# Kernel tuning notes

Hardware: AMD Instinct MI355X
Metric: run time of the kernel (lower is better)

Reference implementation:

```python
import jax, jax.numpy as jnp
import numpy as np
from jax import lax

B, L, DM = 2, 1024, 1024
DIN, DSTATE, DCONV, DTRANK = 2048, 16, 4, 64


def setup_inputs() -> dict:
    key = jax.random.key(0)
    ks = jax.random.split(key, 8)
    s = 0.02
    x = jax.random.normal(ks[0], (B, L, DM), jnp.float32)
    in_proj_w = jax.random.normal(ks[1], (2 * DIN, DM), jnp.float32) * s
    conv_w = jax.random.normal(ks[2], (DIN, 1, DCONV), jnp.float32) * 0.2
    conv_b = jnp.zeros((DIN,), jnp.float32)
    x_proj_w = jax.random.normal(ks[3], (DTRANK + 2 * DSTATE, DIN), jnp.float32) * s
    dt_proj_w = jax.random.normal(ks[4], (DIN, DTRANK), jnp.float32) * s
    dt_proj_b = jnp.full((DIN,), -4.0, jnp.float32)  # small init dt after softplus
    # S4D-real init: A_log = log(1..d_state) per channel
    A_log = jnp.log(jnp.broadcast_to(jnp.arange(1, DSTATE + 1, dtype=jnp.float32), (DIN, DSTATE)))
    D_skip = jnp.ones((DIN,), jnp.float32)
    out_proj_w = jax.random.normal(ks[5], (DM, DIN), jnp.float32) * s
    return {
        "x": x, "norm_w": jnp.ones((DM,), jnp.float32), "norm_b": jnp.zeros((DM,), jnp.float32),
        "in_proj_w": in_proj_w, "conv_w": conv_w, "conv_b": conv_b,
        "x_proj_w": x_proj_w, "dt_proj_w": dt_proj_w, "dt_proj_b": dt_proj_b,
        "A_log": A_log, "D_skip": D_skip, "out_proj_w": out_proj_w,
    }


def _layernorm(x, w, b, eps=1e-5):
    mu = jnp.mean(x, axis=-1, keepdims=True)
    var = jnp.mean(jnp.square(x - mu), axis=-1, keepdims=True)
    return (x - mu) * lax.rsqrt(var + eps) * w + b


def _mamba(h, in_proj_w, conv_w, conv_b, x_proj_w, dt_proj_w, dt_proj_b, A_log, D_skip, out_proj_w):
    # h: [B, L, DM]
    xz = jnp.einsum('bld,ed->ble', h, in_proj_w)          # [B, L, 2*DIN]
    xm, z = jnp.split(xz, 2, axis=-1)                     # each [B, L, DIN]
    # causal depthwise conv1d over time
    xc = jnp.transpose(xm, (0, 2, 1))                     # [B, DIN, L]
    xc = jnp.pad(xc, ((0, 0), (0, 0), (DCONV - 1, 0)))
    xc = lax.conv_general_dilated(xc, conv_w, (1,), 'VALID',
                                  dimension_numbers=('NCH', 'OIH', 'NCH'),
                                  feature_group_count=DIN)
    xc = xc + conv_b[None, :, None]
    xc = jnp.transpose(xc, (0, 2, 1))                     # [B, L, DIN]
    xc = jax.nn.silu(xc)
    # input-dependent SSM parameters
    x_dbl = jnp.einsum('bld,ed->ble', xc, x_proj_w)       # [B, L, DTRANK+2N]
    dt, Bm, Cm = jnp.split(x_dbl, [DTRANK, DTRANK + DSTATE], axis=-1)
    dt = jax.nn.softplus(jnp.einsum('blr,dr->bld', dt, dt_proj_w) + dt_proj_b)  # [B, L, DIN]
    A = -jnp.exp(A_log)                                   # [DIN, N]
    deltaA = jnp.exp(dt[..., None] * A)                   # [B, L, DIN, N]
    deltaBu = dt[..., None] * Bm[:, :, None, :] * xc[..., None]  # [B, L, DIN, N]
    # sequential selective scan over time
    dA_t = jnp.transpose(deltaA, (1, 0, 2, 3))            # [L, B, DIN, N]
    dBu_t = jnp.transpose(deltaBu, (1, 0, 2, 3))
    C_t = jnp.transpose(Cm, (1, 0, 2))                    # [L, B, N]

    def step(hs, inp):
        dA, dBu, Ct = inp
        hs = dA * hs + dBu                                # [B, DIN, N]
        y = jnp.einsum('bdn,bn->bd', hs, Ct)
        return hs, y

    h0 = jnp.zeros((B, DIN, DSTATE), xc.dtype)
    _, ys = lax.scan(step, h0, (dA_t, dBu_t, C_t))        # ys: [L, B, DIN]
    y = jnp.transpose(ys, (1, 0, 2)) + xc * D_skip        # [B, L, DIN]
    y = y * jax.nn.silu(z)
    return jnp.einsum('bld,ed->ble', y, out_proj_w)       # [B, L, DM]


def reference(x, norm_w, norm_b, in_proj_w, conv_w, conv_b, x_proj_w,
              dt_proj_w, dt_proj_b, A_log, D_skip, out_proj_w):
    h = _layernorm(x, norm_w, norm_b)
    return x + _mamba(h, in_proj_w, conv_w, conv_b, x_proj_w,
                      dt_proj_w, dt_proj_b, A_log, D_skip, out_proj_w)
```

## Files before the change

kernel.cpp:

```cpp
#include <hip/hip_runtime.h>


typedef unsigned short u16;
typedef unsigned int u32;

typedef __bf16 bf16x8 __attribute__((ext_vector_type(8)));
typedef float f32x4 __attribute__((ext_vector_type(4)));

#define SCAN_G 32
#define SCAN_T 32
#define NSTATE 65536

#if __has_builtin(__builtin_amdgcn_exp2f)
#define EXP2F(x) __builtin_amdgcn_exp2f(x)
#else
#define EXP2F(x) exp2f(x)
#endif
#define LOG2E 1.44269504f

__device__ __forceinline__ u16 f2bf(float f) {
  u32 u = __float_as_uint(f);
  u32 r = u + 0x7FFFu + ((u >> 16) & 1u);
  return (u16)(r >> 16);
}
__device__ __forceinline__ float bf2f(u16 v) {
  return __uint_as_float(((u32)v) << 16);
}

__device__ __forceinline__ void lds_load16(const u16* g, u16* l) {
  __builtin_amdgcn_global_load_lds(
      (const __attribute__((address_space(1))) u32*)g,
      (__attribute__((address_space(3))) u32*)l, 16, 0, 0);
}

__global__ __launch_bounds__(256) void convert_ln_kernel(
    const float* __restrict__ w0, const float* __restrict__ w1,
    const float* __restrict__ w2, const float* __restrict__ w3,
    u16* __restrict__ o0, u16* __restrict__ o1,
    u16* __restrict__ o2, u16* __restrict__ o3,
    const float* __restrict__ x, const float* __restrict__ nw,
    const float* __restrict__ nb, u16* __restrict__ h) {
  const int bx = blockIdx.x;
  const int tid = threadIdx.x;
  if (bx < 25856) {
    const int i = bx * 256 + tid;
    if (i < 4194304) {
      o0[i] = f2bf(w0[i]);
    } else if (i < 4390912) {
      const int j = i - 4194304;
      o1[j] = f2bf(w1[j]);
    } else if (i < 4521984) {
      const int j = i - 4390912;
      o2[j] = f2bf(w2[j]);
    } else if (i < 6619136) {
      const int j = i - 4521984;
      o3[j] = f2bf(w3[j]);
    }
    return;
  }
  const int row = bx - 25856;
  const float4 v = ((const float4*)(x + (size_t)row * 1024))[tid];
  float s = v.x + v.y + v.z + v.w;
  float s2 = v.x * v.x + v.y * v.y + v.z * v.z + v.w * v.w;
  for (int off = 32; off >= 1; off >>= 1) {
    s += __shfl_xor(s, off);
    s2 += __shfl_xor(s2, off);
  }
  __shared__ float red[8];
  const int wave = tid >> 6;
  if ((tid & 63) == 0) { red[wave * 2] = s; red[wave * 2 + 1] = s2; }
  __syncthreads();
  s = red[0] + red[2] + red[4] + red[6];
  s2 = red[1] + red[3] + red[5] + red[7];
  const float mu = s * (1.0f / 1024.0f);
  const float var = s2 * (1.0f / 1024.0f) - mu * mu;
  const float rstd = rsqrtf(var + 1e-5f);
  const float4 wv = ((const float4*)nw)[tid];
  const float4 bv = ((const float4*)nb)[tid];
  ushort4 o;
  o.x = f2bf((v.x - mu) * rstd * wv.x + bv.x);
  o.y = f2bf((v.y - mu) * rstd * wv.y + bv.y);
  o.z = f2bf((v.z - mu) * rstd * wv.z + bv.z);
  o.w = f2bf((v.w - mu) * rstd * wv.w + bv.w);
  ((ushort4*)(h + (size_t)row * 1024))[tid] = o;
}

__global__ __launch_bounds__(256) void gemm_bt_kernel(
    const u16* __restrict__ A, const u16* __restrict__ W,
    float* __restrict__ C, int M, int N, int K) {
  const int n0 = blockIdx.x * 64;
  const int m0 = blockIdx.y * 64;
  const int ks = blockIdx.z;
  const int kLen = K / 4;
  const int kOff = ks * kLen;
  __shared__ u16 As[64 * 32];
  __shared__ u16 Ws[64 * 32];
  const int tid = threadIdx.x;
  const int wave = tid >> 6;
  const int lane = tid & 63;
  const int wm = (wave >> 1) * 32;
  const int wn = (wave & 1) * 32;
  const int lrow = tid >> 2;
  const int lcg = (tid & 3) * 8;
  const int arow = m0 + lrow;
  const int wrow = n0 + lrow;
  f32x4 acc[2][2];
#pragma unroll
  for (int i = 0; i < 2; ++i)
#pragma unroll
    for (int j = 0; j < 2; ++j) acc[i][j] = (f32x4){0.f, 0.f, 0.f, 0.f};

  const int fm = lane & 15;
  const int fk = (lane >> 4) * 8;

  for (int k0 = kOff; k0 < kOff + kLen; k0 += 32) {
    uint4 av = *(const uint4*)(A + (size_t)arow * K + k0 + lcg);
    uint4 wv = make_uint4(0u, 0u, 0u, 0u);
    if (wrow < N) wv = *(const uint4*)(W + (size_t)wrow * K + k0 + lcg);
    __syncthreads();
    *(uint4*)(As + lrow * 32 + lcg) = av;
    *(uint4*)(Ws + lrow * 32 + lcg) = wv;
    __syncthreads();
    bf16x8 a0 = *(const bf16x8*)(As + (wm + fm) * 32 + fk);
    bf16x8 a1 = *(const bf16x8*)(As + (wm + 16 + fm) * 32 + fk);
    bf16x8 b0 = *(const bf16x8*)(Ws + (wn + fm) * 32 + fk);
    bf16x8 b1 = *(const bf16x8*)(Ws + (wn + 16 + fm) * 32 + fk);
    acc[0][0] = __builtin_amdgcn_mfma_f32_16x16x32_bf16(a0, b0, acc[0][0], 0, 0, 0);
    acc[0][1] = __builtin_amdgcn_mfma_f32_16x16x32_bf16(a0, b1, acc[0][1], 0, 0, 0);
    acc[1][0] = __builtin_amdgcn_mfma_f32_16x16x32_bf16(a1, b0, acc[1][0], 0, 0, 0);
    acc[1][1] = __builtin_amdgcn_mfma_f32_16x16x32_bf16(a1, b1, acc[1][1], 0, 0, 0);
  }

  const int col = lane & 15;
  const int rbase = (lane >> 4) * 4;
#pragma unroll
  for (int tm = 0; tm < 2; ++tm)
#pragma unroll
    for (int tn = 0; tn < 2; ++tn)
#pragma unroll
      for (int r = 0; r < 4; ++r) {
        int m = m0 + wm + tm * 16 + rbase + r;
        int n = n0 + wn + tn * 16 + col;
        if (n < N)
          C[(size_t)ks * M * N + (size_t)m * N + n] = acc[tm][tn][r];
      }
}

__global__ __launch_bounds__(256) void dtgemm_fused_kernel(
    const float* __restrict__ xpart, const u16* __restrict__ Wdt,
    const float* __restrict__ bias, const u16* __restrict__ xcb,
    u32* __restrict__ dxp, float* __restrict__ xdbl) {
  const int N = 2048, K = 64;
  const int n0 = blockIdx.x * 64;
  const int m0 = blockIdx.y * 64;
  const int tid = threadIdx.x;

  if (blockIdx.x == 0) {
#pragma unroll
    for (int j = 0; j < 8; ++j) {
      const int e = tid * 8 + j;
      const int r = e >> 5, c = e & 31;
      const size_t ix = (size_t)(m0 + r) * 96 + 64 + c;
      xdbl[ix] = xpart[ix] + xpart[ix + 196608] + xpart[ix + 2 * 196608] +
                 xpart[ix + 3 * 196608];
    }
  }

  __shared__ u16 As[64 * 32];
  __shared__ u16 Ws[64 * 32];
  const int wave = tid >> 6;
  const int lane = tid & 63;
  const int wm = (wave >> 1) * 32;
  const int wn = (wave & 1) * 32;
  const int lrow = tid >> 2;
  const int lcg = (tid & 3) * 8;
  f32x4 acc[2][2];
#pragma unroll
  for (int i = 0; i < 2; ++i)
#pragma unroll
    for (int j = 0; j < 2; ++j) acc[i][j] = (f32x4){0.f, 0.f, 0.f, 0.f};

  const int fm = lane & 15;
  const int fk = (lane >> 4) * 8;

  for (int k0 = 0; k0 < K; k0 += 32) {
    const size_t ab = (size_t)(m0 + lrow) * 96 + k0 + lcg;
    float av[8];
#pragma unroll
    for (int t = 0; t < 2; ++t) {
      float4 v0 = *(const float4*)&xpart[ab + t * 4];
      float4 v1 = *(const float4*)&xpart[ab + 196608 + t * 4];
      float4 v2 = *(const float4*)&xpart[ab + 2 * 196608 + t * 4];
      float4 v3 = *(const float4*)&xpart[ab + 3 * 196608 + t * 4];
      av[t * 4 + 0] = v0.x + v1.x + v2.x + v3.x;
      av[t * 4 + 1] = v0.y + v1.y + v2.y + v3.y;
      av[t * 4 + 2] = v0.z + v1.z + v2.z + v3.z;
      av[t * 4 + 3] = v0.w + v1.w + v2.w + v3.w;
    }
    ushort4 ap0, ap1;
    ap0.x = f2bf(av[0]); ap0.y = f2bf(av[1]); ap0.z = f2bf(av[2]); ap0.w = f2bf(av[3]);
    ap1.x = f2bf(av[4]); ap1.y = f2bf(av[5]); ap1.z = f2bf(av[6]); ap1.w = f2bf(av[7]);
    uint4 wv = *(const uint4*)(Wdt + (size_t)(n0 + lrow) * K + k0 + lcg);
    __syncthreads();
    *(ushort4*)(As + lrow * 32 + lcg) = ap0;
    *(ushort4*)(As + lrow * 32 + lcg + 4) = ap1;
    *(uint4*)(Ws + lrow * 32 + lcg) = wv;
    __syncthreads();
    bf16x8 a0 = *(const bf16x8*)(As + (wm + fm) * 32 + fk);
    bf16x8 a1 = *(const bf16x8*)(As + (wm + 16 + fm) * 32 + fk);
    bf16x8 b0 = *(const bf16x8*)(Ws + (wn + fm) * 32 + fk);
    bf16x8 b1 = *(const bf16x8*)(Ws + (wn + 16 + fm) * 32 + fk);
    acc[0][0] = __builtin_amdgcn_mfma_f32_16x16x32_bf16(a0, b0, acc[0][0], 0, 0, 0);
    acc[0][1] = __builtin_amdgcn_mfma_f32_16x16x32_bf16(a0, b1, acc[0][1], 0, 0, 0);
    acc[1][0] = __builtin_amdgcn_mfma_f32_16x16x32_bf16(a1, b0, acc[1][0], 0, 0, 0);
    acc[1][1] = __builtin_amdgcn_mfma_f32_16x16x32_bf16(a1, b1, acc[1][1], 0, 0, 0);
  }

  const int col = lane & 15;
  const int rbase = (lane >> 4) * 4;
#pragma unroll
  for (int tm = 0; tm < 2; ++tm)
#pragma unroll
    for (int tn = 0; tn < 2; ++tn)
#pragma unroll
      for (int r = 0; r < 4; ++r) {
        const int m = m0 + wm + tm * 16 + rbase + r;
        const int n = n0 + wn + tn * 16 + col;
        float v = acc[tm][tn][r] + bias[n];
        v = (v > 20.f) ? v : log1pf(__expf(v));
        const u32 xc = xcb[(size_t)m * 2048 + n];
        dxp[(size_t)m * 2048 + n] = (u32)f2bf(v) | (xc << 16);
      }
}

template <int EPI, int SPLITK>
__global__ __launch_bounds__(256) void gemm128_kernel(
    const u16* __restrict__ A, const u16* __restrict__ W,
    u16* __restrict__ Cout, int M, int N, int K) {
  const int n0 = blockIdx.x * 128;
  const int m0 = blockIdx.y * 128;
  const int ks = (SPLITK > 1) ? blockIdx.z : 0;
  const int kLen = K / SPLITK;
  const int k0 = ks * kLen;
  __shared__ u16 As[128 * 32];
  __shared__ u16 Ws[128 * 32];
  const int tid = threadIdx.x;
  const int wave = tid >> 6;
  const int lane = tid & 63;
  const int wm = (wave >> 1) * 64;
  const int wn = (wave & 1) * 64;
  f32x4 acc[4][4];
#pragma unroll
  for (int i = 0; i < 4; ++i)
#pragma unroll
    for (int j = 0; j < 4; ++j) acc[i][j] = (f32x4){0.f, 0.f, 0.f, 0.f};

  const int fm = lane & 15;
  const int fk = (lane >> 4) * 8;
  const int sr = lane >> 2;
  const int sc = (lane & 3) * 8;
  const u16* gA = A + (size_t)(m0 + wave * 32 + sr) * K + k0 + sc;
  const u16* gB = W + (size_t)(n0 + wave * 32 + sr) * K + k0 + sc;
  u16* lA = As + wave * 1024;
  u16* lB = Ws + wave * 1024;

  for (int kk = 0; kk < kLen; kk += 32) {
    __syncthreads();
    lds_load16(gA + kk, lA);
    lds_load16(gA + (size_t)16 * K + kk, lA + 512);
    lds_load16(gB + kk, lB);
    lds_load16(gB + (size_t)16 * K + kk, lB + 512);
    __syncthreads();
    bf16x8 af[4], bfr[4];
#pragma unroll
    for (int i = 0; i < 4; ++i)
      af[i] = *(const bf16x8*)(As + (wm + i * 16 + fm) * 32 + fk);
#pragma unroll
    for (int j = 0; j < 4; ++j)
      bfr[j] = *(const bf16x8*)(Ws + (wn + j * 16 + fm) * 32 + fk);
#pragma unroll
    for (int i = 0; i < 4; ++i)
#pragma unroll
      for (int j = 0; j < 4; ++j)
        acc[i][j] = __builtin_amdgcn_mfma_f32_16x16x32_bf16(af[i], bfr[j], acc[i][j], 0, 0, 0);
  }

  const int col = lane & 15;
  const int rb = (lane >> 4) * 4;
#pragma unroll
  for (int i = 0; i < 4; ++i)
#pragma unroll
    for (int j = 0; j < 4; ++j)
#pragma unroll
      for (int r = 0; r < 4; ++r) {
        const int m = m0 + wm + i * 16 + rb + r;
        const int n = n0 + wn + j * 16 + col;
        if (EPI == 4)
          Cout[(size_t)m * N + n] = f2bf(acc[i][j][r]);
        else
          Cout[(size_t)ks * M * N + (size_t)m * N + n] = f2bf(acc[i][j][r]);
      }
}

__global__ __launch_bounds__(256) void out_comb_kernel(
    const u16* __restrict__ part, const float* __restrict__ x,
    float* __restrict__ out) {
  const int i4 = (blockIdx.x * 256 + threadIdx.x) * 4;
  const float4 xv = *(const float4*)&x[i4];
  float a0 = xv.x, a1 = xv.y, a2 = xv.z, a3 = xv.w;
#pragma unroll
  for (int ks = 0; ks < 4; ++ks) {
    ushort4 pv = *(const ushort4*)&part[(size_t)ks * 2097152 + i4];
    a0 += bf2f(pv.x); a1 += bf2f(pv.y); a2 += bf2f(pv.z); a3 += bf2f(pv.w);
  }
  float4 o = {a0, a1, a2, a3};
  *(float4*)&out[i4] = o;
}

__global__ __launch_bounds__(256) void conv_silu_kernel(
    const u16* __restrict__ xzb, const float* __restrict__ cw,
    const float* __restrict__ cb, u16* __restrict__ xcb) {
  const int idx = blockIdx.x * 256 + threadIdx.x;
  const int d = idx & 2047;
  const int m = idx >> 11;
  const int l = m & 1023;
  const float4 wv = ((const float4*)cw)[d];
  const float w4[4] = {wv.x, wv.y, wv.z, wv.w};
  float acc = cb[d];
#pragma unroll
  for (int k = 0; k < 4; ++k) {
    int lk = l + k - 3;
    if (lk >= 0) acc += bf2f(xzb[(size_t)(m + k - 3) * 4096 + d]) * w4[k];
  }
  const float sv = acc / (1.0f + __expf(-acc));
  xcb[idx] = f2bf(sv);
}

__global__ __launch_bounds__(256) void scan_pass1_kernel(
    const u32* __restrict__ dxp, const float* __restrict__ xdbl,
    const float* __restrict__ A_log, float* __restrict__ hend,
    float* __restrict__ prodA) {
  const int bx = blockIdx.x;
  const int d0 = (bx & 7) * 256;
  const int b = (bx >> 3) & 1;
  const int g = bx >> 4;
  const int tid = threadIdx.x;
  const int d = d0 + tid;
  const int mb = b * 1024 + g * SCAN_T;

  float a2[16];
#pragma unroll
  for (int q = 0; q < 4; ++q) {
    float4 al = *(const float4*)&A_log[(size_t)d * 16 + q * 4];
    a2[q * 4 + 0] = -__expf(al.x) * LOG2E;
    a2[q * 4 + 1] = -__expf(al.y) * LOG2E;
    a2[q * 4 + 2] = -__expf(al.z) * LOG2E;
    a2[q * 4 + 3] = -__expf(al.w) * LOG2E;
  }

  float h[16];
#pragma unroll
  for (int n = 0; n < 16; ++n) h[n] = 0.f;
  float cs = 0.f;

  const u32* dp = dxp + (size_t)mb * 2048 + d;
  const float* xb = xdbl + (size_t)mb * 96 + 64;

#pragma unroll 4
  for (int s = 0; s < SCAN_T; ++s) {
    const u32 u = dp[(size_t)s * 2048];
    const float dtv = __uint_as_float(u << 16);
    const float xcv = __uint_as_float(u & 0xFFFF0000u);
    const float du = dtv * xcv;
    const float4 B0 = *(const float4*)(xb + (size_t)s * 96 + 0);
    const float4 B1 = *(const float4*)(xb + (size_t)s * 96 + 4);
    const float4 B2 = *(const float4*)(xb + (size_t)s * 96 + 8);
    const float4 B3 = *(const float4*)(xb + (size_t)s * 96 + 12);
    const float Bv[16] = {B0.x, B0.y, B0.z, B0.w, B1.x, B1.y, B1.z, B1.w,
                          B2.x, B2.y, B2.z, B2.w, B3.x, B3.y, B3.z, B3.w};
#pragma unroll
    for (int n = 0; n < 16; ++n) {
      const float da = EXP2F(dtv * a2[n]);
      h[n] = __builtin_fmaf(da, h[n], du * Bv[n]);
    }
    cs += dtv;
  }

  const size_t base = ((size_t)(g * 2 + b) * 2048 + d) * 16;
#pragma unroll
  for (int q = 0; q < 4; ++q) {
    float4 hv = {h[q * 4], h[q * 4 + 1], h[q * 4 + 2], h[q * 4 + 3]};
    *(float4*)&hend[base + q * 4] = hv;
    float4 pv = {EXP2F(a2[q * 4] * cs), EXP2F(a2[q * 4 + 1] * cs),
                 EXP2F(a2[q * 4 + 2] * cs), EXP2F(a2[q * 4 + 3] * cs)};
    *(float4*)&prodA[base + q * 4] = pv;
  }
}

__global__ __launch_bounds__(256) void scan_combine_kernel(
    const float* __restrict__ hend, const float* __restrict__ prodA,
    float* __restrict__ hinit) {
  const int sid = blockIdx.x * 256 + threadIdx.x;
  float H = 0.f;
#pragma unroll 8
  for (int g = 0; g < SCAN_G; ++g) {
    hinit[g * NSTATE + sid] = H;
    H = prodA[g * NSTATE + sid] * H + hend[g * NSTATE + sid];
  }
}

__global__ __launch_bounds__(256) void scan_pass2_kernel(
    const u32* __restrict__ dxp, const u16* __restrict__ xzb,
    const float* __restrict__ xdbl, const float* __restrict__ A_log,
    const float* __restrict__ Dsk, const float* __restrict__ hinit,
    u16* __restrict__ yb) {
  const int bx = blockIdx.x;
  const int d0 = (bx & 7) * 256;
  const int b = (bx >> 3) & 1;
  const int g = bx >> 4;
  const int tid = threadIdx.x;
  const int d = d0 + tid;
  const int mb = b * 1024 + g * SCAN_T;

  float a2[16];
#pragma unroll
  for (int q = 0; q < 4; ++q) {
    float4 al = *(const float4*)&A_log[(size_t)d * 16 + q * 4];
    a2[q * 4 + 0] = -__expf(al.x) * LOG2E;
    a2[q * 4 + 1] = -__expf(al.y) * LOG2E;
    a2[q * 4 + 2] = -__expf(al.z) * LOG2E;
    a2[q * 4 + 3] = -__expf(al.w) * LOG2E;
  }
  const float Dd = Dsk[d];

  float h[16];
  {
    const float* hi = hinit + ((size_t)(g * 2 + b) * 2048 + d) * 16;
#pragma unroll
    for (int q = 0; q < 4; ++q) {
      float4 hv = *(const float4*)(hi + q * 4);
      h[q * 4] = hv.x; h[q * 4 + 1] = hv.y; h[q * 4 + 2] = hv.z; h[q * 4 + 3] = hv.w;
    }
  }

  const u32* dp = dxp + (size_t)mb * 2048 + d;
  const u16* zp = xzb + (size_t)mb * 4096 + 2048 + d;
  const float* xb = xdbl + (size_t)mb * 96 + 64;
  u16* yp = yb + (size_t)mb * 2048 + d;

#pragma unroll 2
  for (int s = 0; s < SCAN_T; ++s) {
    const u32 u = dp[(size_t)s * 2048];
    const float dtv = __uint_as_float(u << 16);
    const float xcv = __uint_as_float(u & 0xFFFF0000u);
    const float du = dtv * xcv;
    const float4 B0 = *(const float4*)(xb + (size_t)s * 96 + 0);
    const float4 B1 = *(const float4*)(xb + (size_t)s * 96 + 4);
    const float4 B2 = *(const float4*)(xb + (size_t)s * 96 + 8);
    const float4 B3 = *(const float4*)(xb + (size_t)s * 96 + 12);
    const float4 C0 = *(const float4*)(xb + (size_t)s * 96 + 16);
    const float4 C1 = *(const float4*)(xb + (size_t)s * 96 + 20);
    const float4 C2 = *(const float4*)(xb + (size_t)s * 96 + 24);
    const float4 C3 = *(const float4*)(xb + (size_t)s * 96 + 28);
    const float Bv[16] = {B0.x, B0.y, B0.z, B0.w, B1.x, B1.y, B1.z, B1.w,
                          B2.x, B2.y, B2.z, B2.w, B3.x, B3.y, B3.z, B3.w};
    const float Cv[16] = {C0.x, C0.y, C0.z, C0.w, C1.x, C1.y, C1.z, C1.w,
                          C2.x, C2.y, C2.z, C2.w, C3.x, C3.y, C3.z, C3.w};
    float y = 0.f;
#pragma unroll
    for (int n = 0; n < 16; ++n) {
      const float da = EXP2F(dtv * a2[n]);
      h[n] = __builtin_fmaf(da, h[n], du * Bv[n]);
      y = __builtin_fmaf(h[n], Cv[n], y);
    }
    const float zv = bf2f(zp[(size_t)s * 4096]);
    const float sig = 1.0f / (1.0f + EXP2F(-zv * LOG2E));
    const float yv = (y + xcv * Dd) * (zv * sig);
    yp[(size_t)s * 2048] = f2bf(yv);
  }
}

extern "C" void kernel_launch(void* const* d_in, const int* in_sizes, int n_in,
                              void* d_out, int out_size, void* d_ws, size_t ws_size,
                              hipStream_t stream) {
  const float* x        = (const float*)d_in[0];
  const float* norm_w   = (const float*)d_in[1];
  const float* norm_b   = (const float*)d_in[2];
  const float* in_projw = (const float*)d_in[3];
  const float* conv_w   = (const float*)d_in[4];
  const float* conv_b   = (const float*)d_in[5];
  const float* x_projw  = (const float*)d_in[6];
  const float* dt_projw = (const float*)d_in[7];
  const float* dt_projb = (const float*)d_in[8];
  const float* A_log    = (const float*)d_in[9];
  const float* D_skip   = (const float*)d_in[10];
  const float* out_projw= (const float*)d_in[11];
  float* out = (float*)d_out;

  char* p = (char*)d_ws;
  auto alloc = [&](size_t bytes) {
    char* r = p;
    p += (bytes + 255) & ~(size_t)255;
    return r;
  };
  u16* xzb    = (u16*)alloc(2048ULL * 4096 * 2);
  u16* xcb    = (u16*)alloc(2048ULL * 2048 * 2);
  u32* dxp    = (u32*)alloc(2048ULL * 2048 * 4);
  float* xdbl = (float*)alloc(2048ULL * 96 * 4);
  u16* h_bf   = (u16*)alloc(2048ULL * 1024 * 2);
  u16* ybf    = (u16*)alloc(2048ULL * 2048 * 2);
  u16* Wi     = (u16*)alloc(4096ULL * 1024 * 2);
  u16* Wx     = (u16*)alloc(96ULL * 2048 * 2);
  u16* Wdt    = (u16*)alloc(2048ULL * 64 * 2);
  u16* Wo     = (u16*)alloc(1024ULL * 2048 * 2);
  float* hend = (float*)alloc((size_t)SCAN_G * NSTATE * 4);
  float* prodA= (float*)alloc((size_t)SCAN_G * NSTATE * 4);
  float* hinit= (float*)alloc((size_t)SCAN_G * NSTATE * 4);
  float* xpart= (float*)alloc(4ULL * 2048 * 96 * 4);
  u16* opart  = xzb;
  (void)ws_size; (void)in_sizes; (void)n_in; (void)out_size;

  convert_ln_kernel<<<27904, 256, 0, stream>>>(in_projw, x_projw, dt_projw,
                                               out_projw, Wi, Wx, Wdt, Wo,
                                               x, norm_w, norm_b, h_bf);

  gemm128_kernel<4, 1><<<dim3(32, 16), 256, 0, stream>>>(h_bf, Wi, xzb, 2048, 4096, 1024);

  conv_silu_kernel<<<16384, 256, 0, stream>>>(xzb, conv_w, conv_b, xcb);

  gemm_bt_kernel<<<dim3(2, 32, 4), 256, 0, stream>>>(xcb, Wx, xpart, 2048, 96, 2048);

  dtgemm_fused_kernel<<<dim3(32, 32), 256, 0, stream>>>(xpart, Wdt, dt_projb,
                                                        xcb, dxp, xdbl);

  scan_pass1_kernel<<<512, 256, 0, stream>>>(dxp, xdbl, A_log, hend, prodA);
  scan_combine_kernel<<<256, 256, 0, stream>>>(hend, prodA, hinit);
  scan_pass2_kernel<<<512, 256, 0, stream>>>(dxp, xzb, xdbl, A_log, D_skip,
                                             hinit, ybf);

  gemm128_kernel<3, 4><<<dim3(8, 16, 4), 256, 0, stream>>>(ybf, Wo, opart, 2048, 1024, 2048);
  out_comb_kernel<<<2048, 256, 0, stream>>>(opart, x, out);
}
```

Baseline: 243.9 us.

## Vectorize weight conversion, unpack dt/xc buffers, fuse out-proj with residual add

The weight-conversion blocks now handle four floats per thread with float4 loads and ushort4 stores, which cuts the block count. The packed dt/xc u32 buffer is replaced by a separate bf16 dt buffer, and the scan reads xc directly from the existing conv output. The split-K out-projection, its bf16 partials and the separate combine kernel are replaced by a single 64x128-tile GEMM that adds the residual x in its epilogue. This removes one launch and the partial-sum round trip through memory, but the scan now issues two separate 2-byte loads per step and the out GEMM runs without split-K parallelism (256 blocks).

```diff
diff --git a/kernel.cpp b/kernel.cpp
--- a/kernel.cpp
+++ b/kernel.cpp
@@ -42,23 +42,22 @@
     const float* __restrict__ nb, u16* __restrict__ h) {
   const int bx = blockIdx.x;
   const int tid = threadIdx.x;
-  if (bx < 25856) {
-    const int i = bx * 256 + tid;
-    if (i < 4194304) {
-      o0[i] = f2bf(w0[i]);
-    } else if (i < 4390912) {
-      const int j = i - 4194304;
-      o1[j] = f2bf(w1[j]);
-    } else if (i < 4521984) {
-      const int j = i - 4390912;
-      o2[j] = f2bf(w2[j]);
-    } else if (i < 6619136) {
-      const int j = i - 4521984;
-      o3[j] = f2bf(w3[j]);
-    }
+  if (bx < 6464) {
+    const int q = bx * 256 + tid;
+    const float4* src;
+    ushort4* dst;
+    int off;
+    if (q < 1048576) { src = (const float4*)w0; dst = (ushort4*)o0; off = q; }
+    else if (q < 1097728) { src = (const float4*)w1; dst = (ushort4*)o1; off = q - 1048576; }
+    else if (q < 1130496) { src = (const float4*)w2; dst = (ushort4*)o2; off = q - 1097728; }
+    else { src = (const float4*)w3; dst = (ushort4*)o3; off = q - 1130496; }
+    const float4 v = src[off];
+    ushort4 o;
+    o.x = f2bf(v.x); o.y = f2bf(v.y); o.z = f2bf(v.z); o.w = f2bf(v.w);
+    dst[off] = o;
     return;
   }
-  const int row = bx - 25856;
+  const int row = bx - 6464;
   const float4 v = ((const float4*)(x + (size_t)row * 1024))[tid];
   float s = v.x + v.y + v.z + v.w;
   float s2 = v.x * v.x + v.y * v.y + v.z * v.z + v.w * v.w;
@@ -85,6 +84,85 @@
   ((ushort4*)(h + (size_t)row * 1024))[tid] = o;
 }
 
+__global__ __launch_bounds__(256) void gemm128_kernel(
+    const u16* __restrict__ A, const u16* __restrict__ W,
+    u16* __restrict__ Cout, int M, int N, int K) {
+  const int n0 = blockIdx.x * 128;
+  const int m0 = blockIdx.y * 128;
+  __shared__ u16 As[128 * 32];
+  __shared__ u16 Ws[128 * 32];
+  const int tid = threadIdx.x;
+  const int wave = tid >> 6;
+  const int lane = tid & 63;
+  const int wm = (wave >> 1) * 64;
+  const int wn = (wave & 1) * 64;
+  f32x4 acc[4][4];
+#pragma unroll
+  for (int i = 0; i < 4; ++i)
+#pragma unroll
+    for (int j = 0; j < 4; ++j) acc[i][j] = (f32x4){0.f, 0.f, 0.f, 0.f};
+  const int fm = lane & 15;
+  const int fk = (lane >> 4) * 8;
+  const int sr = lane >> 2;
+  const int sc = (lane & 3) * 8;
+  const u16* gA = A + (size_t)(m0 + wave * 32 + sr) * K + sc;
+  const u16* gB = W + (size_t)(n0 + wave * 32 + sr) * K + sc;
+  u16* lA = As + wave * 1024;
+  u16* lB = Ws + wave * 1024;
+
+  for (int kk = 0; kk < K; kk += 32) {
+    __syncthreads();
+    lds_load16(gA + kk, lA);
+    lds_load16(gA + (size_t)16 * K + kk, lA + 512);
+    lds_load16(gB + kk, lB);
+    lds_load16(gB + (size_t)16 * K + kk, lB + 512);
+    __syncthreads();
+    bf16x8 af[4], bfr[4];
+#pragma unroll
+    for (int i = 0; i < 4; ++i)
+      af[i] = *(const bf16x8*)(As + (wm + i * 16 + fm) * 32 + fk);
+#pragma unroll
+    for (int j = 0; j < 4; ++j)
+      bfr[j] = *(const bf16x8*)(Ws + (wn + j * 16 + fm) * 32 + fk);
+#pragma unroll
+    for (int i = 0; i < 4; ++i)
+#pragma unroll
+      for (int j = 0; j < 4; ++j)
+        acc[i][j] = __builtin_amdgcn_mfma_f32_16x16x32_bf16(af[i], bfr[j], acc[i][j], 0, 0, 0);
+  }
+  const int col = lane & 15;
+  const int rb = (lane >> 4) * 4;
+#pragma unroll
+  for (int i = 0; i < 4; ++i)
+#pragma unroll
+    for (int j = 0; j < 4; ++j)
+#pragma unroll
+      for (int r = 0; r < 4; ++r) {
+        const int m = m0 + wm + i * 16 + rb + r;
+        const int n = n0 + wn + j * 16 + col;
+        Cout[(size_t)m * N + n] = f2bf(acc[i][j][r]);
+      }
+}
+
+__global__ __launch_bounds__(256) void conv_silu_kernel(
+    const u16* __restrict__ xzb, const float* __restrict__ cw,
+    const float* __restrict__ cb, u16* __restrict__ xcb) {
+  const int idx = blockIdx.x * 256 + threadIdx.x;
+  const int d = idx & 2047;
+  const int m = idx >> 11;
+  const int l = m & 1023;
+  const float4 wv = ((const float4*)cw)[d];
+  const float w4[4] = {wv.x, wv.y, wv.z, wv.w};
+  float acc = cb[d];
+#pragma unroll
+  for (int k = 0; k < 4; ++k) {
+    int lk = l + k - 3;
+    if (lk >= 0) acc += bf2f(xzb[(size_t)(m + k - 3) * 4096 + d]) * w4[k];
+  }
+  const float sv = acc / (1.0f + __expf(-acc));
+  xcb[idx] = f2bf(sv);
+}
+
 __global__ __launch_bounds__(256) void gemm_bt_kernel(
     const u16* __restrict__ A, const u16* __restrict__ W,
     float* __restrict__ C, int M, int N, int K) {
@@ -102,19 +180,16 @@
   const int wn = (wave & 1) * 32;
   const int lrow = tid >> 2;
   const int lcg = (tid & 3) * 8;
-  const int arow = m0 + lrow;
-  const int wrow = n0 + lrow;
   f32x4 acc[2][2];
 #pragma unroll
   for (int i = 0; i < 2; ++i)
 #pragma unroll
     for (int j = 0; j < 2; ++j) acc[i][j] = (f32x4){0.f, 0.f, 0.f, 0.f};
-
   const int fm = lane & 15;
   const int fk = (lane >> 4) * 8;
-
+  const int wrow = n0 + lrow;
   for (int k0 = kOff; k0 < kOff + kLen; k0 += 32) {
-    uint4 av = *(const uint4*)(A + (size_t)arow * K + k0 + lcg);
+    uint4 av = *(const uint4*)(A + (size_t)(m0 + lrow) * K + k0 + lcg);
     uint4 wv = make_uint4(0u, 0u, 0u, 0u);
     if (wrow < N) wv = *(const uint4*)(W + (size_t)wrow * K + k0 + lcg);
     __syncthreads();
@@ -130,7 +205,6 @@
     acc[1][0] = __builtin_amdgcn_mfma_f32_16x16x32_bf16(a1, b0, acc[1][0], 0, 0, 0);
     acc[1][1] = __builtin_amdgcn_mfma_f32_16x16x32_bf16(a1, b1, acc[1][1], 0, 0, 0);
   }
-
   const int col = lane & 15;
   const int rbase = (lane >> 4) * 4;
 #pragma unroll
@@ -148,24 +222,21 @@
 
 __global__ __launch_bounds__(256) void dtgemm_fused_kernel(
     const float* __restrict__ xpart, const u16* __restrict__ Wdt,
-    const float* __restrict__ bias, const u16* __restrict__ xcb,
-    u32* __restrict__ dxp, float* __restrict__ xdbl) {
+    const float* __restrict__ bias, u16* __restrict__ dtb,
+    float* __restrict__ xdbl) {
   const int N = 2048, K = 64;
   const int n0 = blockIdx.x * 64;
   const int m0 = blockIdx.y * 64;
   const int tid = threadIdx.x;
-
   if (blockIdx.x == 0) {
 #pragma unroll
     for (int j = 0; j < 8; ++j) {
       const int e = tid * 8 + j;
-      const int r = e >> 5, c = e & 31;
-      const size_t ix = (size_t)(m0 + r) * 96 + 64 + c;
+      const size_t ix = (size_t)(m0 + (e >> 5)) * 96 + 64 + (e & 31);
       xdbl[ix] = xpart[ix] + xpart[ix + 196608] + xpart[ix + 2 * 196608] +
                  xpart[ix + 3 * 196608];
     }
   }
-
   __shared__ u16 As[64 * 32];
   __shared__ u16 Ws[64 * 32];
   const int wave = tid >> 6;
@@ -179,10 +250,8 @@
   for (int i = 0; i < 2; ++i)
 #pragma unroll
     for (int j = 0; j < 2; ++j) acc[i][j] = (f32x4){0.f, 0.f, 0.f, 0.f};
-
   const int fm = lane & 15;
   const int fk = (lane >> 4) * 8;
-
   for (int k0 = 0; k0 < K; k0 += 32) {
     const size_t ab = (size_t)(m0 + lrow) * 96 + k0 + lcg;
     float av[8];
@@ -215,7 +284,6 @@
     acc[1][0] = __builtin_amdgcn_mfma_f32_16x16x32_bf16(a1, b0, acc[1][0], 0, 0, 0);
     acc[1][1] = __builtin_amdgcn_mfma_f32_16x16x32_bf16(a1, b1, acc[1][1], 0, 0, 0);
   }
-
   const int col = lane & 15;
   const int rbase = (lane >> 4) * 4;
 #pragma unroll
@@ -228,118 +296,14 @@
         const int n = n0 + wn + tn * 16 + col;
         float v = acc[tm][tn][r] + bias[n];
         v = (v > 20.f) ? v : log1pf(__expf(v));
-        const u32 xc = xcb[(size_t)m * 2048 + n];
-        dxp[(size_t)m * 2048 + n] = (u32)f2bf(v) | (xc << 16);
+        dtb[(size_t)m * 2048 + n] = f2bf(v);
       }
 }
 
-template <int EPI, int SPLITK>
-__global__ __launch_bounds__(256) void gemm128_kernel(
-    const u16* __restrict__ A, const u16* __restrict__ W,
-    u16* __restrict__ Cout, int M, int N, int K) {
-  const int n0 = blockIdx.x * 128;
-  const int m0 = blockIdx.y * 128;
-  const int ks = (SPLITK > 1) ? blockIdx.z : 0;
-  const int kLen = K / SPLITK;
-  const int k0 = ks * kLen;
-  __shared__ u16 As[128 * 32];
-  __shared__ u16 Ws[128 * 32];
-  const int tid = threadIdx.x;
-  const int wave = tid >> 6;
-  const int lane = tid & 63;
-  const int wm = (wave >> 1) * 64;
-  const int wn = (wave & 1) * 64;
-  f32x4 acc[4][4];
-#pragma unroll
-  for (int i = 0; i < 4; ++i)
-#pragma unroll
-    for (int j = 0; j < 4; ++j) acc[i][j] = (f32x4){0.f, 0.f, 0.f, 0.f};
-
-  const int fm = lane & 15;
-  const int fk = (lane >> 4) * 8;
-  const int sr = lane >> 2;
-  const int sc = (lane & 3) * 8;
-  const u16* gA = A + (size_t)(m0 + wave * 32 + sr) * K + k0 + sc;
-  const u16* gB = W + (size_t)(n0 + wave * 32 + sr) * K + k0 + sc;
-  u16* lA = As + wave * 1024;
-  u16* lB = Ws + wave * 1024;
-
-  for (int kk = 0; kk < kLen; kk += 32) {
-    __syncthreads();
-    lds_load16(gA + kk, lA);
-    lds_load16(gA + (size_t)16 * K + kk, lA + 512);
-    lds_load16(gB + kk, lB);
-    lds_load16(gB + (size_t)16 * K + kk, lB + 512);
-    __syncthreads();
-    bf16x8 af[4], bfr[4];
-#pragma unroll
-    for (int i = 0; i < 4; ++i)
-      af[i] = *(const bf16x8*)(As + (wm + i * 16 + fm) * 32 + fk);
-#pragma unroll
-    for (int j = 0; j < 4; ++j)
-      bfr[j] = *(const bf16x8*)(Ws + (wn + j * 16 + fm) * 32 + fk);
-#pragma unroll
-    for (int i = 0; i < 4; ++i)
-#pragma unroll
-      for (int j = 0; j < 4; ++j)
-        acc[i][j] = __builtin_amdgcn_mfma_f32_16x16x32_bf16(af[i], bfr[j], acc[i][j], 0, 0, 0);
-  }
-
-  const int col = lane & 15;
-  const int rb = (lane >> 4) * 4;
-#pragma unroll
-  for (int i = 0; i < 4; ++i)
-#pragma unroll
-    for (int j = 0; j < 4; ++j)
-#pragma unroll
-      for (int r = 0; r < 4; ++r) {
-        const int m = m0 + wm + i * 16 + rb + r;
-        const int n = n0 + wn + j * 16 + col;
-        if (EPI == 4)
-          Cout[(size_t)m * N + n] = f2bf(acc[i][j][r]);
-        else
-          Cout[(size_t)ks * M * N + (size_t)m * N + n] = f2bf(acc[i][j][r]);
-      }
-}
-
-__global__ __launch_bounds__(256) void out_comb_kernel(
-    const u16* __restrict__ part, const float* __restrict__ x,
-    float* __restrict__ out) {
-  const int i4 = (blockIdx.x * 256 + threadIdx.x) * 4;
-  const float4 xv = *(const float4*)&x[i4];
-  float a0 = xv.x, a1 = xv.y, a2 = xv.z, a3 = xv.w;
-#pragma unroll
-  for (int ks = 0; ks < 4; ++ks) {
-    ushort4 pv = *(const ushort4*)&part[(size_t)ks * 2097152 + i4];
-    a0 += bf2f(pv.x); a1 += bf2f(pv.y); a2 += bf2f(pv.z); a3 += bf2f(pv.w);
-  }
-  float4 o = {a0, a1, a2, a3};
-  *(float4*)&out[i4] = o;
-}
-
-__global__ __launch_bounds__(256) void conv_silu_kernel(
-    const u16* __restrict__ xzb, const float* __restrict__ cw,
-    const float* __restrict__ cb, u16* __restrict__ xcb) {
-  const int idx = blockIdx.x * 256 + threadIdx.x;
-  const int d = idx & 2047;
-  const int m = idx >> 11;
-  const int l = m & 1023;
-  const float4 wv = ((const float4*)cw)[d];
-  const float w4[4] = {wv.x, wv.y, wv.z, wv.w};
-  float acc = cb[d];
-#pragma unroll
-  for (int k = 0; k < 4; ++k) {
-    int lk = l + k - 3;
-    if (lk >= 0) acc += bf2f(xzb[(size_t)(m + k - 3) * 4096 + d]) * w4[k];
-  }
-  const float sv = acc / (1.0f + __expf(-acc));
-  xcb[idx] = f2bf(sv);
-}
-
 __global__ __launch_bounds__(256) void scan_pass1_kernel(
-    const u32* __restrict__ dxp, const float* __restrict__ xdbl,
-    const float* __restrict__ A_log, float* __restrict__ hend,
-    float* __restrict__ prodA) {
+    const u16* __restrict__ dtb, const u16* __restrict__ xcb,
+    const float* __restrict__ xdbl, const float* __restrict__ A_log,
+    float* __restrict__ hend, float* __restrict__ prodA) {
   const int bx = blockIdx.x;
   const int d0 = (bx & 7) * 256;
   const int b = (bx >> 3) & 1;
@@ -347,7 +311,6 @@
   const int tid = threadIdx.x;
   const int d = d0 + tid;
   const int mb = b * 1024 + g * SCAN_T;
-
   float a2[16];
 #pragma unroll
   for (int q = 0; q < 4; ++q) {
@@ -357,20 +320,17 @@
     a2[q * 4 + 2] = -__expf(al.z) * LOG2E;
     a2[q * 4 + 3] = -__expf(al.w) * LOG2E;
   }
-
   float h[16];
 #pragma unroll
   for (int n = 0; n < 16; ++n) h[n] = 0.f;
   float cs = 0.f;
-
-  const u32* dp = dxp + (size_t)mb * 2048 + d;
+  const u16* dp = dtb + (size_t)mb * 2048 + d;
+  const u16* xp = xcb + (size_t)mb * 2048 + d;
   const float* xb = xdbl + (size_t)mb * 96 + 64;
-
 #pragma unroll 4
   for (int s = 0; s < SCAN_T; ++s) {
-    const u32 u = dp[(size_t)s * 2048];
-    const float dtv = __uint_as_float(u << 16);
-    const float xcv = __uint_as_float(u & 0xFFFF0000u);
+    const float dtv = bf2f(dp[(size_t)s * 2048]);
+    const float xcv = bf2f(xp[(size_t)s * 2048]);
     const float du = dtv * xcv;
     const float4 B0 = *(const float4*)(xb + (size_t)s * 96 + 0);
     const float4 B1 = *(const float4*)(xb + (size_t)s * 96 + 4);
@@ -385,7 +345,6 @@
     }
     cs += dtv;
   }
-
   const size_t base = ((size_t)(g * 2 + b) * 2048 + d) * 16;
 #pragma unroll
   for (int q = 0; q < 4; ++q) {
@@ -410,10 +369,10 @@
 }
 
 __global__ __launch_bounds__(256) void scan_pass2_kernel(
-    const u32* __restrict__ dxp, const u16* __restrict__ xzb,
-    const float* __restrict__ xdbl, const float* __restrict__ A_log,
-    const float* __restrict__ Dsk, const float* __restrict__ hinit,
-    u16* __restrict__ yb) {
+    const u16* __restrict__ dtb, const u16* __restrict__ xcb,
+    const u16* __restrict__ xzb, const float* __restrict__ xdbl,
+    const float* __restrict__ A_log, const float* __restrict__ Dsk,
+    const float* __restrict__ hinit, u16* __restrict__ yb) {
   const int bx = blockIdx.x;
   const int d0 = (bx & 7) * 256;
   const int b = (bx >> 3) & 1;
@@ -421,7 +380,6 @@
   const int tid = threadIdx.x;
   const int d = d0 + tid;
   const int mb = b * 1024 + g * SCAN_T;
-
   float a2[16];
 #pragma unroll
   for (int q = 0; q < 4; ++q) {
@@ -432,7 +390,6 @@
     a2[q * 4 + 3] = -__expf(al.w) * LOG2E;
   }
   const float Dd = Dsk[d];
-
   float h[16];
   {
     const float* hi = hinit + ((size_t)(g * 2 + b) * 2048 + d) * 16;
@@ -442,17 +399,15 @@
       h[q * 4] = hv.x; h[q * 4 + 1] = hv.y; h[q * 4 + 2] = hv.z; h[q * 4 + 3] = hv.w;
     }
   }
-
-  const u32* dp = dxp + (size_t)mb * 2048 + d;
+  const u16* dp = dtb + (size_t)mb * 2048 + d;
+  const u16* xp = xcb + (size_t)mb * 2048 + d;
   const u16* zp = xzb + (size_t)mb * 4096 + 2048 + d;
   const float* xb = xdbl + (size_t)mb * 96 + 64;
   u16* yp = yb + (size_t)mb * 2048 + d;
-
 #pragma unroll 2
   for (int s = 0; s < SCAN_T; ++s) {
-    const u32 u = dp[(size_t)s * 2048];
-    const float dtv = __uint_as_float(u << 16);
-    const float xcv = __uint_as_float(u & 0xFFFF0000u);
+    const float dtv = bf2f(dp[(size_t)s * 2048]);
+    const float xcv = bf2f(xp[(size_t)s * 2048]);
     const float du = dtv * xcv;
     const float4 B0 = *(const float4*)(xb + (size_t)s * 96 + 0);
     const float4 B1 = *(const float4*)(xb + (size_t)s * 96 + 4);
@@ -478,6 +433,66 @@
     const float yv = (y + xcv * Dd) * (zv * sig);
     yp[(size_t)s * 2048] = f2bf(yv);
   }
+}
+
+__global__ __launch_bounds__(256) void gemm_out_kernel(
+    const u16* __restrict__ A, const u16* __restrict__ W,
+    const float* __restrict__ x, float* __restrict__ out) {
+  const int K = 2048;
+  const int n0 = blockIdx.x * 128;
+  const int m0 = blockIdx.y * 64;
+  __shared__ u16 As[64 * 32];
+  __shared__ u16 Ws[128 * 32];
+  const int tid = threadIdx.x;
+  const int wave = tid >> 6;
+  const int lane = tid & 63;
+  const int wm = (wave >> 1) * 32;
+  const int wn = (wave & 1) * 64;
+  f32x4 acc[2][4];
+#pragma unroll
+  for (int i = 0; i < 2; ++i)
+#pragma unroll
+    for (int j = 0; j < 4; ++j) acc[i][j] = (f32x4){0.f, 0.f, 0.f, 0.f};
+  const int fm = lane & 15;
+  const int fk = (lane >> 4) * 8;
+  const int sr = lane >> 2;
+  const int sc = (lane & 3) * 8;
+  const u16* gA = A + (size_t)(m0 + wave * 16 + sr) * K + sc;
+  const u16* gB = W + (size_t)(n0 + wave * 32 + sr) * K + sc;
+  u16* lA = As + wave * 512;
+  u16* lB = Ws + wave * 1024;
+
+  for (int kk = 0; kk < K; kk += 32) {
+    __syncthreads();
+    lds_load16(gA + kk, lA);
+    lds_load16(gB + kk, lB);
+    lds_load16(gB + (size_t)16 * K + kk, lB + 512);
+    __syncthreads();
+    bf16x8 af[2], bfr[4];
+#pragma unroll
+    for (int i = 0; i < 2; ++i)
+      af[i] = *(const bf16x8*)(As + (wm + i * 16 + fm) * 32 + fk);
+#pragma unroll
+    for (int j = 0; j < 4; ++j)
+      bfr[j] = *(const bf16x8*)(Ws + (wn + j * 16 + fm) * 32 + fk);
+#pragma unroll
+    for (int i = 0; i < 2; ++i)
+#pragma unroll
+      for (int j = 0; j < 4; ++j)
+        acc[i][j] = __builtin_amdgcn_mfma_f32_16x16x32_bf16(af[i], bfr[j], acc[i][j], 0, 0, 0);
+  }
+  const int col = lane & 15;
+  const int rb = (lane >> 4) * 4;
+#pragma unroll
+  for (int i = 0; i < 2; ++i)
+#pragma unroll
+    for (int j = 0; j < 4; ++j)
+#pragma unroll
+      for (int r = 0; r < 4; ++r) {
+        const int m = m0 + wm + i * 16 + rb + r;
+        const int n = n0 + wn + j * 16 + col;
+        out[(size_t)m * 1024 + n] = x[(size_t)m * 1024 + n] + acc[i][j][r];
+      }
 }
 
 extern "C" void kernel_launch(void* const* d_in, const int* in_sizes, int n_in,
@@ -505,7 +520,7 @@
   };
   u16* xzb    = (u16*)alloc(2048ULL * 4096 * 2);
   u16* xcb    = (u16*)alloc(2048ULL * 2048 * 2);
-  u32* dxp    = (u32*)alloc(2048ULL * 2048 * 4);
+  u16* dtb16  = (u16*)alloc(2048ULL * 2048 * 2);
   float* xdbl = (float*)alloc(2048ULL * 96 * 4);
   u16* h_bf   = (u16*)alloc(2048ULL * 1024 * 2);
   u16* ybf    = (u16*)alloc(2048ULL * 2048 * 2);
@@ -517,27 +532,25 @@
   float* prodA= (float*)alloc((size_t)SCAN_G * NSTATE * 4);
   float* hinit= (float*)alloc((size_t)SCAN_G * NSTATE * 4);
   float* xpart= (float*)alloc(4ULL * 2048 * 96 * 4);
-  u16* opart  = xzb;
   (void)ws_size; (void)in_sizes; (void)n_in; (void)out_size;
 
-  convert_ln_kernel<<<27904, 256, 0, stream>>>(in_projw, x_projw, dt_projw,
-                                               out_projw, Wi, Wx, Wdt, Wo,
-                                               x, norm_w, norm_b, h_bf);
-
-  gemm128_kernel<4, 1><<<dim3(32, 16), 256, 0, stream>>>(h_bf, Wi, xzb, 2048, 4096, 1024);
+  convert_ln_kernel<<<8512, 256, 0, stream>>>(in_projw, x_projw, dt_projw,
+                                              out_projw, Wi, Wx, Wdt, Wo,
+                                              x, norm_w, norm_b, h_bf);
+
+  gemm128_kernel<<<dim3(32, 16), 256, 0, stream>>>(h_bf, Wi, xzb, 2048, 4096, 1024);
 
   conv_silu_kernel<<<16384, 256, 0, stream>>>(xzb, conv_w, conv_b, xcb);
 
   gemm_bt_kernel<<<dim3(2, 32, 4), 256, 0, stream>>>(xcb, Wx, xpart, 2048, 96, 2048);
 
   dtgemm_fused_kernel<<<dim3(32, 32), 256, 0, stream>>>(xpart, Wdt, dt_projb,
-                                                        xcb, dxp, xdbl);
-
-  scan_pass1_kernel<<<512, 256, 0, stream>>>(dxp, xdbl, A_log, hend, prodA);
+                                                        dtb16, xdbl);
+
+  scan_pass1_kernel<<<512, 256, 0, stream>>>(dtb16, xcb, xdbl, A_log, hend, prodA);
   scan_combine_kernel<<<256, 256, 0, stream>>>(hend, prodA, hinit);
-  scan_pass2_kernel<<<512, 256, 0, stream>>>(dxp, xzb, xdbl, A_log, D_skip,
-                                             hinit, ybf);
-
-  gemm128_kernel<3, 4><<<dim3(8, 16, 4), 256, 0, stream>>>(ybf, Wo, opart, 2048, 1024, 2048);
-  out_comb_kernel<<<2048, 256, 0, stream>>>(opart, x, out);
-}
+  scan_pass2_kernel<<<512, 256, 0, stream>>>(dtb16, xcb, xzb, xdbl, A_log,
+                                             D_skip, hinit, ybf);
+
+  gemm_out_kernel<<<dim3(8, 32), 256, 0, stream>>>(ybf, Wo, x, out);
+}
```

Measured after the change: 246.5 us. Within noise of the previous version (+1.1%).
